# Kernel optimization log

Measured on AMD Instinct MI355X. Metric: run time of the kernel, lower is better.

## Reference

```python
import jax, jax.numpy as jnp
import numpy as np
from jax import lax

D = 384      # embd_d
L = 4        # num_blocks
B = 64
SHW, THW = 24, 12
NS, NT = SHW * SHW, THW * THW   # 576, 144
EPS = 1e-5


def _ln(x, g, b):
    mu = jnp.mean(x, axis=-1, keepdims=True)
    var = jnp.mean(jnp.square(x - mu), axis=-1, keepdims=True)
    return (x - mu) * lax.rsqrt(var + EPS) * g + b


def setup_inputs() -> dict:
    key = jax.random.key(0)
    ks = iter(jax.random.split(key, 64))
    f32 = jnp.float32
    def nrm(shape, s=0.02):
        return jax.random.normal(next(ks), shape, dtype=f32) * s
    inp = {
        'search': jax.random.normal(next(ks), (B, NS, D), dtype=f32),
        'target': jax.random.normal(next(ks), (B, NT, D), dtype=f32),
        # learned tokens / positional params
        'cls': nrm((1, 1, D), 1.0),
        'search_pos': nrm((1, NS, D), 0.5),
        'target_pos': nrm((1, NT, D), 0.5),
        # stacked per-block params [L, ...]
        'ln1_g': jnp.ones((L, D), f32), 'ln1_b': jnp.zeros((L, D), f32),
        'Wq': nrm((L, D, D)), 'bq': jnp.zeros((L, D), f32),
        'Wk': nrm((L, D, D)), 'bk': jnp.zeros((L, D), f32),
        'Wv': nrm((L, D, D)), 'bv': jnp.zeros((L, D), f32),
        'ln2_g': jnp.ones((L, D), f32), 'ln2_b': jnp.zeros((L, D), f32),
        'W1': nrm((L, D, 2 * D)), 'b1': jnp.zeros((L, 2 * D), f32),
        'W2': nrm((L, 2 * D, D)), 'b2': jnp.zeros((L, D), f32),
        # head
        'lnf_g': jnp.ones((D,), f32), 'lnf_b': jnp.zeros((D,), f32),
        'Wl1': nrm((D, D)), 'bl1': jnp.zeros((D,), f32),
        'Wl2': nrm((D, 1)), 'bl2': jnp.zeros((1,), f32),
    }
    return inp


def reference(search, target, cls, search_pos, target_pos,
              ln1_g, ln1_b, Wq, bq, Wk, bk, Wv, bv,
              ln2_g, ln2_b, W1, b1, W2, b2,
              lnf_g, lnf_b, Wl1, bl1, Wl2, bl2):
    scale = D ** (-0.5)  # note: full embed dim, as in source
    x = jnp.concatenate([
        jnp.broadcast_to(cls, (B, 1, D)),
        search + search_pos,
        target + target_pos,
    ], axis=1)  # [B, 1+Ns+Nt, D]

    def block(x, p):
        l1g, l1b, wq, bq_, wk, bk_, wv, bv_, l2g, l2b, w1, b1_, w2, b2_ = p
        y = _ln(x, l1g, l1b)
        q = y @ wq + bq_
        k = y @ wk + bk_
        v = y @ wv + bv_
        attn = jax.nn.softmax(jnp.einsum('bid,bjd->bij', q, k) * scale, axis=-1)
        x = x + jnp.einsum('bij,bjd->bid', attn, v)
        h = _ln(x, l2g, l2b)
        x = x + (jax.nn.gelu(h @ w1 + b1_, approximate=False) @ w2 + b2_)
        return x, None

    x, _ = lax.scan(block, x, (ln1_g, ln1_b, Wq, bq, Wk, bk, Wv, bv,
                               ln2_g, ln2_b, W1, b1, W2, b2))
    h = _ln(x[:, 0], lnf_g, lnf_b)          # cls token [B, D]
    h = jax.nn.relu(h @ Wl1 + bl1)
    return h @ Wl2 + bl2                     # [B, 1]
```

## Files before the change

### kernel.cpp

```cpp
#include <hip/hip_runtime.h>
#include <hip/hip_bf16.h>
#include <math.h>

#define DD 384
#define NBATCH 64
#define NSEQ 721
#define NROWS (NBATCH*NSEQ)
#define NLAYER 4

typedef __bf16 bf16_t;
typedef __bf16 bf16x8 __attribute__((ext_vector_type(8)));
typedef float  f32x4  __attribute__((ext_vector_type(4)));

static __device__ __forceinline__ void split_bf16(float v, bf16_t& h, bf16_t& l) {
    h = (bf16_t)v;
    l = (bf16_t)(v - (float)h);
}
static __device__ __forceinline__ bf16x8 bzero8() {
    bf16x8 v = {(bf16_t)0.f,(bf16_t)0.f,(bf16_t)0.f,(bf16_t)0.f,
                (bf16_t)0.f,(bf16_t)0.f,(bf16_t)0.f,(bf16_t)0.f};
    return v;
}
static __device__ __forceinline__ void gload16(const void* g, void* l) {
    __builtin_amdgcn_global_load_lds(
        (const __attribute__((address_space(1))) unsigned int*)g,
        (__attribute__((address_space(3))) unsigned int*)l, 16, 0, 0);
}
static __device__ __forceinline__ int xcd_swz(int nwg) {
    int orig = blockIdx.x;
    int q = nwg >> 3, r = nwg & 7;
    int xcd = orig & 7, within = orig >> 3;
    int base = (xcd < r) ? xcd*(q+1) : r*(q+1) + (xcd - r)*q;
    return base + within;
}
static __device__ __forceinline__ void ln_from_partials(const float* ss, const float* ss2,
                                                        int row, float& mu, float& rstd) {
    float s = 0.f, q2 = 0.f;
    #pragma unroll
    for (int k = 0; k < 6; ++k) { s += ss[k*NROWS + row]; q2 += ss2[k*NROWS + row]; }
    mu = s * (1.f/DD);
    float var = q2 * (1.f/DD) - mu*mu;
    rstd = rsqrtf(var + 1e-5f);
}

__global__ __launch_bounds__(256) void build_x_kernel(const float* __restrict__ search,
                               const float* __restrict__ target,
                               const float* __restrict__ cls,
                               const float* __restrict__ spos,
                               const float* __restrict__ tpos,
                               bf16_t* __restrict__ xh, bf16_t* __restrict__ xl,
                               float* __restrict__ wss, float* __restrict__ wss2) {
    int wave = threadIdx.x >> 6, lane = threadIdx.x & 63;
    int row = blockIdx.x * 4 + wave;
    if (row >= NROWS) return;
    int b = row / NSEQ, n = row % NSEQ;
    float s = 0.f, q2 = 0.f;
    #pragma unroll
    for (int i = 0; i < 6; ++i) {
        int d = lane + 64*i;
        float val;
        if (n == 0)        val = cls[d];
        else if (n <= 576) val = search[((size_t)b*576 + (n-1))*DD + d] + spos[(size_t)(n-1)*DD + d];
        else               val = target[((size_t)b*144 + (n-577))*DD + d] + tpos[(size_t)(n-577)*DD + d];
        bf16_t h, l;
        split_bf16(val, h, l);
        xh[(size_t)row*DD + d] = h;
        xl[(size_t)row*DD + d] = l;
        s += val; q2 += val*val;
    }
    #pragma unroll
    for (int m = 1; m < 64; m <<= 1) { s += __shfl_xor(s, m); q2 += __shfl_xor(q2, m); }
    if (lane == 0) {
        wss[row] = s; wss2[row] = q2;
        #pragma unroll
        for (int k = 1; k < 6; ++k) { wss[k*NROWS + row] = 0.f; wss2[k*NROWS + row] = 0.f; }
    }
}

__global__ void transpose_split_kernel(const float* __restrict__ src,
                                       const float* __restrict__ g,
                                       bf16_t* __restrict__ dh,
                                       bf16_t* __restrict__ dl,
                                       int K, int N) {
    int idx = blockIdx.x * blockDim.x + threadIdx.x;
    if (idx >= K*N) return;
    int k = idx / N, n = idx % N;
    float v = src[idx];
    if (g) v *= g[k];
    bf16_t h, l;
    split_bf16(v, h, l);
    dh[(size_t)n*K + k] = h;
    dl[(size_t)n*K + k] = l;
}

__global__ void colsum_kernel(const float* __restrict__ W, const float* __restrict__ g,
                              const float* __restrict__ b, const float* __restrict__ bias,
                              float* __restrict__ c1, float* __restrict__ c2,
                              int K, int N, int outStride, int outOff) {
    int l = blockIdx.y;
    int n = blockIdx.x * 256 + threadIdx.x;
    if (n >= N) return;
    const float* Wl = W + (size_t)l*K*N;
    const float* gl = g + (size_t)l*K;
    const float* bl = b + (size_t)l*K;
    float s1 = 0.f, s2 = 0.f;
    for (int k = 0; k < K; ++k) {
        float w = Wl[(size_t)k*N + n];
        s1 = fmaf(gl[k], w, s1);
        s2 = fmaf(bl[k], w, s2);
    }
    c1[(size_t)l*outStride + outOff + n] = s1;
    c2[(size_t)l*outStride + outOff + n] = s2 + bias[(size_t)l*N + n];
}

static __device__ __forceinline__ void gemm_core(
        const bf16_t* __restrict__ ah, const bf16_t* __restrict__ al,
        const bf16_t* __restrict__ bh, const bf16_t* __restrict__ bl,
        bf16_t (&ls)[32][64][8],
        int m0, int n0, int K, f32x4 (&acc)[4][4]) {
    int t = threadIdx.x;
    int w = t >> 6, lane = t & 63;
    int c = lane & 15, g = lane >> 4;
    int wr = w >> 1, wc = w & 1;
    const bf16_t* src0 = (w==0) ? ah : (w==1) ? al : (w==2) ? bh : bl;
    int base_rc = (w < 2) ? m0 : n0;
    const bf16_t* srcbase = src0 + (size_t)(base_rc + c)*K + 8*g;

    int ksteps = K >> 5;
    for (int kt = 0; kt < ksteps; ++kt) {
        int k0 = kt << 5;
        __syncthreads();
        #pragma unroll
        for (int i = 0; i < 8; ++i)
            gload16(srcbase + (size_t)(16*i)*K + k0, &ls[w*8 + i][0][0]);
        __syncthreads();
        bf16x8 af_h[4], af_l[4], bf_h[4], bf_l[4];
        #pragma unroll
        for (int i = 0; i < 4; ++i) {
            af_h[i] = *(const bf16x8*)&ls[     4*wr + i][lane][0];
            af_l[i] = *(const bf16x8*)&ls[ 8 + 4*wr + i][lane][0];
            bf_h[i] = *(const bf16x8*)&ls[16 + 4*wc + i][lane][0];
            bf_l[i] = *(const bf16x8*)&ls[24 + 4*wc + i][lane][0];
        }
        #pragma unroll
        for (int i = 0; i < 4; ++i)
            #pragma unroll
            for (int j = 0; j < 4; ++j) {
                acc[i][j] = __builtin_amdgcn_mfma_f32_16x16x32_bf16(af_h[i], bf_h[j], acc[i][j], 0,0,0);
                acc[i][j] = __builtin_amdgcn_mfma_f32_16x16x32_bf16(af_h[i], bf_l[j], acc[i][j], 0,0,0);
                acc[i][j] = __builtin_amdgcn_mfma_f32_16x16x32_bf16(af_l[i], bf_h[j], acc[i][j], 0,0,0);
            }
    }
}

__global__ __launch_bounds__(256, 4) void gemm_qkv(
        const bf16_t* __restrict__ ah, const bf16_t* __restrict__ al,
        const bf16_t* __restrict__ bh, const bf16_t* __restrict__ bl,
        const float* __restrict__ ss, const float* __restrict__ ss2,
        const float* __restrict__ c1, const float* __restrict__ c2,
        bf16_t* __restrict__ qout, bf16_t* __restrict__ kout,
        bf16_t* __restrict__ vth, bf16_t* __restrict__ vtl,
        int M, int MP, int nwg) {
    __shared__ __align__(16) bf16_t ls[32][64][8];
    int wgid = xcd_swz(nwg);
    int m0 = (wgid / 9) * 128, n0 = (wgid % 9) * 128;
    f32x4 zero4 = {0.f,0.f,0.f,0.f};
    f32x4 acc[4][4];
    #pragma unroll
    for (int i = 0; i < 4; ++i)
        #pragma unroll
        for (int j = 0; j < 4; ++j) acc[i][j] = zero4;
    gemm_core(ah, al, bh, bl, ls, m0, n0, DD, acc);

    int t = threadIdx.x, w = t >> 6, lane = t & 63;
    int c = lane & 15, g = lane >> 4;
    int wr = w >> 1, wc = w & 1;
    float rmu[16], rrs[16];
    #pragma unroll
    for (int i = 0; i < 4; ++i)
        #pragma unroll
        for (int r = 0; r < 4; ++r) {
            int row = m0 + 64*wr + 16*i + 4*g + r;
            float mu = 0.f, rstd = 1.f;
            if (row < M) ln_from_partials(ss, ss2, row, mu, rstd);
            rmu[i*4+r] = mu; rrs[i*4+r] = rstd;
        }
    int seg = n0 / 384;
    if (seg < 2) {
        bf16_t* outb = (seg == 0) ? qout : kout;
        int segoff = seg * 384;
        #pragma unroll
        for (int j = 0; j < 4; ++j) {
            int nglob = n0 + 64*wc + 16*j + c;
            int nloc = nglob - segoff;
            float C1 = c1[nglob], C2 = c2[nglob];
            #pragma unroll
            for (int i = 0; i < 4; ++i) {
                int rbase = m0 + 64*wr + 16*i + 4*g;
                #pragma unroll
                for (int r = 0; r < 4; ++r) {
                    int row = rbase + r;
                    if (row >= M) continue;
                    float val = rrs[i*4+r]*(acc[i][j][r] - rmu[i*4+r]*C1) + C2;
                    outb[(size_t)row*DD + nloc] = (bf16_t)val;
                }
            }
        }
    } else {
        int vbase = n0 - 768;
        bool tail = (m0 + 128 > M);
        if (!tail) {
            bf16_t* LST = &ls[0][0][0];
            #pragma unroll
            for (int pass = 0; pass < 2; ++pass) {
                __syncthreads();
                #pragma unroll
                for (int j = 0; j < 4; ++j) {
                    int d = 64*wc + 16*j + c;
                    int nglob = 768 + vbase + 0; (void)nglob;
                    float C1 = c1[n0 + 64*wc + 16*j + c];
                    float C2 = c2[n0 + 64*wc + 16*j + c];
                    #pragma unroll
                    for (int i = 0; i < 4; ++i)
                        #pragma unroll
                        for (int r = 0; r < 4; ++r) {
                            int tok = 64*wr + 16*i + 4*g + r;
                            float val = rrs[i*4+r]*(acc[i][j][r] - rmu[i*4+r]*C1) + C2;
                            bf16_t h, l;
                            split_bf16(val, h, l);
                            LST[d*128 + (tok ^ ((d & 15) << 3))] = pass ? l : h;
                        }
                }
                __syncthreads();
                bf16_t* outp = pass ? vtl : vth;
                #pragma unroll
                for (int p = 0; p < 8; ++p) {
                    int chunk = t + 256*p;
                    int d = chunk >> 4;
                    int tok0 = (chunk & 15) * 8;
                    uint4 v = *(const uint4*)&LST[d*128 + (tok0 ^ ((d & 15) << 3))];
                    *(uint4*)(outp + (size_t)(vbase + d)*MP + m0 + tok0) = v;
                }
            }
        } else {
            #pragma unroll
            for (int j = 0; j < 4; ++j) {
                int d = vbase + 64*wc + 16*j + c;
                float C1 = c1[n0 + 64*wc + 16*j + c];
                float C2 = c2[n0 + 64*wc + 16*j + c];
                #pragma unroll
                for (int i = 0; i < 4; ++i) {
                    int rbase = m0 + 64*wr + 16*i + 4*g;
                    #pragma unroll
                    for (int r = 0; r < 4; ++r) {
                        int row = rbase + r;
                        if (row >= M) continue;
                        float val = rrs[i*4+r]*(acc[i][j][r] - rmu[i*4+r]*C1) + C2;
                        bf16_t h, l;
                        split_bf16(val, h, l);
                        size_t o = (size_t)d*MP + row;
                        vth[o] = h;
                        vtl[o] = l;
                    }
                }
            }
        }
    }
}

template<int EPI, int NT>
__global__ __launch_bounds__(256, 4) void gemm_mfma(
        const bf16_t* __restrict__ ah, const bf16_t* __restrict__ al,
        const bf16_t* __restrict__ bh, const bf16_t* __restrict__ bl,
        const float* __restrict__ ss, const float* __restrict__ ss2,
        const float* __restrict__ c1, const float* __restrict__ c2,
        const float* __restrict__ bias,
        const bf16_t* __restrict__ resh, const bf16_t* __restrict__ resl,
        bf16_t* __restrict__ o1, bf16_t* __restrict__ o2,
        float* __restrict__ wss, float* __restrict__ wss2,
        int M, int N, int K, int nwg) {
    __shared__ __align__(16) bf16_t ls[32][64][8];
    int wgid = xcd_swz(nwg);
    int m0 = (wgid / NT) * 128, n0 = (wgid % NT) * 128;
    f32x4 zero4 = {0.f,0.f,0.f,0.f};
    f32x4 acc[4][4];
    #pragma unroll
    for (int i = 0; i < 4; ++i)
        #pragma unroll
        for (int j = 0; j < 4; ++j) acc[i][j] = zero4;
    gemm_core(ah, al, bh, bl, ls, m0, n0, K, acc);

    int t = threadIdx.x, w = t >> 6, lane = t & 63;
    int c = lane & 15, g = lane >> 4;
    int wr = w >> 1, wc = w & 1;

    if (EPI == 2) {
        float rmu[16], rrs[16];
        #pragma unroll
        for (int i = 0; i < 4; ++i)
            #pragma unroll
            for (int r = 0; r < 4; ++r) {
                int row = m0 + 64*wr + 16*i + 4*g + r;
                float mu = 0.f, rstd = 1.f;
                if (row < M) ln_from_partials(ss, ss2, row, mu, rstd);
                rmu[i*4+r] = mu; rrs[i*4+r] = rstd;
            }
        #pragma unroll
        for (int j = 0; j < 4; ++j) {
            int n = n0 + 64*wc + 16*j + c;
            float C1 = c1[n], C2 = c2[n];
            #pragma unroll
            for (int i = 0; i < 4; ++i) {
                int rbase = m0 + 64*wr + 16*i + 4*g;
                #pragma unroll
                for (int r = 0; r < 4; ++r) {
                    int row = rbase + r;
                    if (row >= M) continue;
                    float val = rrs[i*4+r]*(acc[i][j][r] - rmu[i*4+r]*C1) + C2;
                    val = 0.5f*val*(1.0f + erff(val*0.70710678118654752f));
                    bf16_t h, l;
                    split_bf16(val, h, l);
                    size_t o = (size_t)row*N + n;
                    o1[o] = h;
                    o2[o] = l;
                }
            }
        }
    } else {
        int slot = (wgid % NT) + 3*wc;
        #pragma unroll
        for (int i = 0; i < 4; ++i)
            #pragma unroll
            for (int r = 0; r < 4; ++r) {
                int row = m0 + 64*wr + 16*i + 4*g + r;
                if (row >= M) continue;
                float s = 0.f, q2 = 0.f;
                #pragma unroll
                for (int j = 0; j < 4; ++j) {
                    int n = n0 + 64*wc + 16*j + c;
                    size_t o = (size_t)row*N + n;
                    float val = acc[i][j][r] + bias[n] + (float)resh[o] + (float)resl[o];
                    bf16_t h, l;
                    split_bf16(val, h, l);
                    o1[o] = h;
                    o2[o] = l;
                    s += val; q2 += val*val;
                }
                #pragma unroll
                for (int m = 1; m < 16; m <<= 1) { s += __shfl_xor(s, m); q2 += __shfl_xor(q2, m); }
                if (c == 0) {
                    wss[slot*NROWS + row] = s;
                    wss2[slot*NROWS + row] = q2;
                }
            }
    }
}

__global__ __launch_bounds__(256, 2) void attn_mfma(
        const bf16_t* __restrict__ qh, const bf16_t* __restrict__ kh,
        const bf16_t* __restrict__ vth, const bf16_t* __restrict__ vtl,
        bf16_t* __restrict__ xh, bf16_t* __restrict__ xl,
        float* __restrict__ wss, float* __restrict__ wss2, int MP, int nwg) {
    __shared__ __align__(16) char smem[73728];
    bf16_t* kf = (bf16_t*)smem;
    char* vhp = smem + 24576;
    char* vlp = smem + 49152;

    int t = threadIdx.x, w = t >> 6, lane = t & 63;
    int c = lane & 15, g = lane >> 4;
    int wgid = xcd_swz(nwg);
    int bl_ = wgid / 12;
    int q0 = (wgid % 12) * 64;
    size_t bb = (size_t)bl_ * NSEQ;
    int qrow = q0 + 16*w + c;
    bool qok = (qrow < NSEQ);
    const float scale = 0.05103103630798287f;
    int vswz = (c ^ (c >> 2)) & 3;
    int dma_dd  = lane >> 2;
    int dma_kv8 = (lane & 3) ^ ((dma_dd ^ (dma_dd >> 2)) & 3);

    bf16x8 qf[12];
    #pragma unroll
    for (int ks = 0; ks < 12; ++ks) {
        if (qok) qf[ks] = *(const bf16x8*)(qh + (bb + qrow)*DD + 32*ks + 8*g);
        else     qf[ks] = bzero8();
    }

    f32x4 zero4 = {0.f,0.f,0.f,0.f};
    f32x4 oacc[24];
    #pragma unroll
    for (int i = 0; i < 24; ++i) oacc[i] = zero4;
    float m_run = -1e30f, l_run = 0.f;

    #pragma unroll
    for (int i = 0; i < 6; ++i) {
        int s = i*4 + w;
        int ks = s >> 1, mf = s & 1;
        gload16(kh + (bb + (size_t)(16*mf + c))*DD + 32*ks + 8*g, kf + s*512);
    }

    for (int kt = 0; kt < 23; ++kt) {
        int kv0 = kt * 32;
        asm volatile("s_waitcnt vmcnt(0)" ::: "memory");
        __builtin_amdgcn_s_barrier();
        #pragma unroll
        for (int i = 0; i < 6; ++i) {
            int s = i*4 + w;
            size_t gro = (size_t)(16*s + dma_dd)*MP + bb + kv0 + 8*dma_kv8;
            gload16(vth + gro, (bf16_t*)vhp + s*512);
            gload16(vtl + gro, (bf16_t*)vlp + s*512);
        }
        f32x4 sacc[2];
        sacc[0] = zero4; sacc[1] = zero4;
        #pragma unroll
        for (int ks = 0; ks < 12; ++ks) {
            bf16x8 a0 = *(const bf16x8*)(kf + ((size_t)(2*ks+0)*64 + lane)*8);
            bf16x8 a1 = *(const bf16x8*)(kf + ((size_t)(2*ks+1)*64 + lane)*8);
            sacc[0] = __builtin_amdgcn_mfma_f32_16x16x32_bf16(a0, qf[ks], sacc[0], 0,0,0);
            sacc[1] = __builtin_amdgcn_mfma_f32_16x16x32_bf16(a1, qf[ks], sacc[1], 0,0,0);
        }
        float p[2][4];
        float mx = -1e30f;
        #pragma unroll
        for (int mf = 0; mf < 2; ++mf)
            #pragma unroll
            for (int r = 0; r < 4; ++r) {
                float sv = sacc[mf][r] * scale;
                int kv = kv0 + 16*mf + 4*g + r;
                if (kv >= NSEQ) sv = -1e30f;
                p[mf][r] = sv;
                mx = fmaxf(mx, sv);
            }
        mx = fmaxf(mx, __shfl_xor(mx, 16));
        mx = fmaxf(mx, __shfl_xor(mx, 32));
        float m_new = fmaxf(m_run, mx);
        float corr = __expf(m_run - m_new);
        float psum = 0.f;
        #pragma unroll
        for (int mf = 0; mf < 2; ++mf)
            #pragma unroll
            for (int r = 0; r < 4; ++r) {
                float pv = __expf(p[mf][r] - m_new);
                p[mf][r] = pv;
                psum += pv;
            }
        psum += __shfl_xor(psum, 16);
        psum += __shfl_xor(psum, 32);
        l_run = l_run * corr + psum;
        m_run = m_new;
        #pragma unroll
        for (int i = 0; i < 24; ++i) oacc[i] *= corr;
        bf16x8 ph, pl;
        #pragma unroll
        for (int mf = 0; mf < 2; ++mf)
            #pragma unroll
            for (int r = 0; r < 4; ++r) {
                bf16_t hh, ll;
                split_bf16(p[mf][r], hh, ll);
                ph[mf*4 + r] = hh;
                pl[mf*4 + r] = ll;
            }
        asm volatile("s_waitcnt vmcnt(0)" ::: "memory");
        __builtin_amdgcn_s_barrier();
        if (kt + 1 < 23) {
            int kv0n = kv0 + 32;
            #pragma unroll
            for (int i = 0; i < 6; ++i) {
                int s = i*4 + w;
                int ks = s >> 1, mf = s & 1;
                gload16(kh + (bb + (size_t)(kv0n + 16*mf + c))*DD + 32*ks + 8*g, kf + s*512);
            }
        }
        #pragma unroll
        for (int mf = 0; mf < 24; ++mf) {
            int dr = 16*mf + c;
            const char* vb  = vhp + dr*64;
            const char* vb2 = vlp + dr*64;
            int o0 = ((((g>>1)     ^ vswz) << 4) | (8*(g&1)));
            int o1 = (((2 + (g>>1)) ^ vswz) << 4) | (8*(g&1));
            union { uint2 u[2]; bf16x8 v; } va, vc2;
            va.u[0]  = *(const uint2*)(vb  + o0);
            va.u[1]  = *(const uint2*)(vb  + o1);
            vc2.u[0] = *(const uint2*)(vb2 + o0);
            vc2.u[1] = *(const uint2*)(vb2 + o1);
            oacc[mf] = __builtin_amdgcn_mfma_f32_16x16x32_bf16(va.v,  ph, oacc[mf], 0,0,0);
            oacc[mf] = __builtin_amdgcn_mfma_f32_16x16x32_bf16(va.v,  pl, oacc[mf], 0,0,0);
            oacc[mf] = __builtin_amdgcn_mfma_f32_16x16x32_bf16(vc2.v, ph, oacc[mf], 0,0,0);
        }
    }
    float inv = 1.f / l_run;
    float s = 0.f, q2 = 0.f;
    if (qok) {
        bf16_t* xhr = xh + (bb + qrow)*DD;
        bf16_t* xlr = xl + (bb + qrow)*DD;
        #pragma unroll
        for (int mf = 0; mf < 24; ++mf)
            #pragma unroll
            for (int r = 0; r < 4; ++r) {
                int d = 16*mf + 4*g + r;
                float xv = (float)xhr[d] + (float)xlr[d] + oacc[mf][r]*inv;
                bf16_t h, l;
                split_bf16(xv, h, l);
                xhr[d] = h;
                xlr[d] = l;
                s += xv; q2 += xv*xv;
            }
    }
    s += __shfl_xor(s, 16);  q2 += __shfl_xor(q2, 16);
    s += __shfl_xor(s, 32);  q2 += __shfl_xor(q2, 32);
    if (qok && g == 0) {
        int rowL = bl_*NSEQ + qrow;
        wss[rowL] = s; wss2[rowL] = q2;
        #pragma unroll
        for (int k = 1; k < 6; ++k) { wss[k*NROWS + rowL] = 0.f; wss2[k*NROWS + rowL] = 0.f; }
    }
}

__global__ __launch_bounds__(384) void head_kernel(const bf16_t* __restrict__ xh,
    const bf16_t* __restrict__ xl,
    const float* __restrict__ g, const float* __restrict__ bb,
    const float* __restrict__ Wl1, const float* __restrict__ bl1,
    const float* __restrict__ Wl2, const float* __restrict__ bl2,
    float* __restrict__ outp) {
    __shared__ float yv[384];
    __shared__ float r1[6], r2[6], r3[6];
    int b = blockIdx.x, t = threadIdx.x;
    size_t o = (size_t)b*NSEQ*DD + t;
    float v = (float)xh[o] + (float)xl[o];
    float s = v;
    #pragma unroll
    for (int m = 1; m < 64; m <<= 1) s += __shfl_xor(s, m);
    if ((t & 63) == 0) r1[t>>6] = s;
    __syncthreads();
    float mu = (r1[0]+r1[1]+r1[2]+r1[3]+r1[4]+r1[5]) * (1.f/384.f);
    float dd = v - mu;
    float sq = dd*dd;
    #pragma unroll
    for (int m = 1; m < 64; m <<= 1) sq += __shfl_xor(sq, m);
    if ((t & 63) == 0) r2[t>>6] = sq;
    __syncthreads();
    float var = (r2[0]+r2[1]+r2[2]+r2[3]+r2[4]+r2[5]) * (1.f/384.f);
    float rstd = rsqrtf(var + 1e-5f);
    yv[t] = dd*rstd*g[t] + bb[t];
    __syncthreads();
    float acc = bl1[t];
    for (int d2 = 0; d2 < 384; d2++) acc = fmaf(yv[d2], Wl1[d2*384 + t], acc);
    acc = fmaxf(acc, 0.f);
    float oo = acc * Wl2[t];
    #pragma unroll
    for (int m = 1; m < 64; m <<= 1) oo += __shfl_xor(oo, m);
    if ((t & 63) == 0) r3[t>>6] = oo;
    __syncthreads();
    if (t == 0) outp[b] = r3[0]+r3[1]+r3[2]+r3[3]+r3[4]+r3[5] + bl2[0];
}

extern "C" void kernel_launch(void* const* d_in, const int* in_sizes, int n_in,
                              void* d_out, int out_size, void* d_ws, size_t ws_size,
                              hipStream_t stream) {
    const float* search = (const float*)d_in[0];
    const float* target = (const float*)d_in[1];
    const float* cls    = (const float*)d_in[2];
    const float* spos   = (const float*)d_in[3];
    const float* tpos   = (const float*)d_in[4];
    const float* ln1_g  = (const float*)d_in[5];
    const float* ln1_b  = (const float*)d_in[6];
    const float* Wq     = (const float*)d_in[7];
    const float* bq     = (const float*)d_in[8];
    const float* Wk     = (const float*)d_in[9];
    const float* bk     = (const float*)d_in[10];
    const float* Wv     = (const float*)d_in[11];
    const float* bv     = (const float*)d_in[12];
    const float* ln2_g  = (const float*)d_in[13];
    const float* ln2_b  = (const float*)d_in[14];
    const float* W1     = (const float*)d_in[15];
    const float* b1     = (const float*)d_in[16];
    const float* W2     = (const float*)d_in[17];
    const float* b2     = (const float*)d_in[18];
    const float* lnf_g  = (const float*)d_in[19];
    const float* lnf_b  = (const float*)d_in[20];
    const float* Wl1    = (const float*)d_in[21];
    const float* bl1    = (const float*)d_in[22];
    const float* Wl2    = (const float*)d_in[23];
    const float* bl2    = (const float*)d_in[24];

    size_t off = 0;
    char* base = (char*)d_ws;
    auto alloc = [&](size_t bytes) -> void* {
        void* p = base + off;
        off += (bytes + 255) & ~(size_t)255;
        return p;
    };

    bf16_t* xh = (bf16_t*)alloc((size_t)NROWS * DD * 2);
    bf16_t* xl = (bf16_t*)alloc((size_t)NROWS * DD * 2);
    float* ssum  = (float*)alloc((size_t)6*NROWS*4);
    float* ssum2 = (float*)alloc((size_t)6*NROWS*4);

    const int SQKV = 1152*DD;
    const int SM = DD*768;
    bf16_t* wqkvh = (bf16_t*)alloc((size_t)4*SQKV*2);
    bf16_t* wqkvl = (bf16_t*)alloc((size_t)4*SQKV*2);
    bf16_t* w1h = (bf16_t*)alloc((size_t)4*SM*2);
    bf16_t* w1l = (bf16_t*)alloc((size_t)4*SM*2);
    bf16_t* w2h = (bf16_t*)alloc((size_t)4*SM*2);
    bf16_t* w2l = (bf16_t*)alloc((size_t)4*SM*2);
    float* cqkv1 = (float*)alloc((size_t)4*1152*4);
    float* cqkv2 = (float*)alloc((size_t)4*1152*4);
    float* cm11  = (float*)alloc((size_t)4*768*4);
    float* cm12  = (float*)alloc((size_t)4*768*4);

    const size_t qB  = (size_t)NSEQ*DD*2;
    const size_t mB  = (size_t)NSEQ*768*2;
    const size_t perB = 2*qB + 4*(size_t)DD*NSEQ + 4096;
    size_t avail = (ws_size > off + 262144) ? (ws_size - off - 262144) : 0;
    int G = (int)(avail / perB);
    if (G > NBATCH) G = NBATCH;
    if (G < 1) G = 1;

    int MPi = (int)((((size_t)G*NSEQ + 7) & ~(size_t)7) + 32);
    size_t vBytes = (size_t)DD * MPi * 2;
    size_t sizeQKV = 2*qB*(size_t)G + 2*vBytes;
    size_t sizeMid = 2*mB*(size_t)G;
    size_t Usz = (sizeQKV > sizeMid ? sizeQKV : sizeMid);

    char* U = (char*)alloc(Usz);
    bf16_t* qhB  = (bf16_t*)U;
    bf16_t* khB  = (bf16_t*)(U + qB*G);
    bf16_t* vth  = (bf16_t*)(U + 2*qB*G);
    bf16_t* vtl  = (bf16_t*)(U + 2*qB*G + vBytes);
    bf16_t* midh = (bf16_t*)U;
    bf16_t* midl = (bf16_t*)(U + mB*G);

    build_x_kernel<<<(NROWS+3)/4, 256, 0, stream>>>(search, target, cls, spos, tpos,
                                                    xh, xl, ssum, ssum2);

    const int SQ = DD*DD;
    for (int l = 0; l < NLAYER; ++l) {
        bf16_t* dsth = wqkvh + (size_t)l*SQKV;
        bf16_t* dstl = wqkvl + (size_t)l*SQKV;
        transpose_split_kernel<<<(SQ+255)/256, 256, 0, stream>>>(Wq + (size_t)l*SQ, ln1_g + l*DD, dsth,          dstl,          DD, DD);
        transpose_split_kernel<<<(SQ+255)/256, 256, 0, stream>>>(Wk + (size_t)l*SQ, ln1_g + l*DD, dsth + 384*DD, dstl + 384*DD, DD, DD);
        transpose_split_kernel<<<(SQ+255)/256, 256, 0, stream>>>(Wv + (size_t)l*SQ, ln1_g + l*DD, dsth + 768*DD, dstl + 768*DD, DD, DD);
        transpose_split_kernel<<<(SM+255)/256, 256, 0, stream>>>(W1 + (size_t)l*SM, ln2_g + l*DD, w1h + (size_t)l*SM, w1l + (size_t)l*SM, DD, 768);
        transpose_split_kernel<<<(SM+255)/256, 256, 0, stream>>>(W2 + (size_t)l*SM, nullptr,      w2h + (size_t)l*SM, w2l + (size_t)l*SM, 768, DD);
    }
    colsum_kernel<<<dim3(2, NLAYER), 256, 0, stream>>>(Wq, ln1_g, ln1_b, bq, cqkv1, cqkv2, DD, DD, 1152, 0);
    colsum_kernel<<<dim3(2, NLAYER), 256, 0, stream>>>(Wk, ln1_g, ln1_b, bk, cqkv1, cqkv2, DD, DD, 1152, 384);
    colsum_kernel<<<dim3(2, NLAYER), 256, 0, stream>>>(Wv, ln1_g, ln1_b, bv, cqkv1, cqkv2, DD, DD, 1152, 768);
    colsum_kernel<<<dim3(3, NLAYER), 256, 0, stream>>>(W1, ln2_g, ln2_b, b1, cm11, cm12, DD, 768, 768, 0);

    for (int l = 0; l < NLAYER; ++l) {
        for (int b0 = 0; b0 < NBATCH; b0 += G) {
            int cb = (NBATCH - b0 < G) ? (NBATCH - b0) : G;
            int Mc = cb * NSEQ;
            bf16_t* xch = xh + (size_t)b0 * NSEQ * DD;
            bf16_t* xcl = xl + (size_t)b0 * NSEQ * DD;
            float* ssc  = ssum  + (size_t)b0 * NSEQ;
            float* ssc2 = ssum2 + (size_t)b0 * NSEQ;
            int mtiles = (Mc + 127)/128;
            int nwgQKV = 9*mtiles, nwgM1 = 6*mtiles, nwgM2 = 3*mtiles, nwgA = 12*cb;

            gemm_qkv<<<nwgQKV, 256, 0, stream>>>(xch, xcl,
                    wqkvh + (size_t)l*SQKV, wqkvl + (size_t)l*SQKV,
                    ssc, ssc2, cqkv1 + l*1152, cqkv2 + l*1152,
                    qhB, khB, vth, vtl, Mc, MPi, nwgQKV);
            attn_mfma<<<nwgA, 256, 0, stream>>>(qhB, khB, vth, vtl, xch, xcl,
                    ssc, ssc2, MPi, nwgA);
            gemm_mfma<2,6><<<nwgM1, 256, 0, stream>>>(xch, xcl,
                    w1h + (size_t)l*SM, w1l + (size_t)l*SM,
                    ssc, ssc2, cm11 + l*768, cm12 + l*768, nullptr,
                    nullptr, nullptr, midh, midl, nullptr, nullptr, Mc, 768, DD, nwgM1);
            gemm_mfma<3,3><<<nwgM2, 256, 0, stream>>>(midh, midl,
                    w2h + (size_t)l*SM, w2l + (size_t)l*SM,
                    nullptr, nullptr, nullptr, nullptr, b2 + l*DD,
                    xch, xcl, xch, xcl, ssc, ssc2, Mc, DD, 768, nwgM2);
        }
    }
    head_kernel<<<NBATCH, 384, 0, stream>>>(xh, xl, lnf_g, lnf_b, Wl1, bl1, Wl2, bl2, (float*)d_out);
}
```

Measured before the change: 4.044 ms.

## Tile QKV GEMM per batch and store V transposed per batch

The QKV GEMM now tiles the M dimension per batch element, using 6 tiles of 128 tokens over 721 tokens, and writes V transposed into a per-batch [DD][736] layout with zeroed padding. The old layout used one global transposed V with stride MP. Every tile now takes the coalesced LDS-transpose store path, and attention reads V using per-batch offsets. The cost is that per-batch tiles (768 rows for 721 tokens) do some wasted GEMM work, and the mid buffer sizing now relies on perB*G being large enough.

```diff
diff --git a/kernel.cpp b/kernel.cpp
--- a/kernel.cpp
+++ b/kernel.cpp
@@ -7,6 +7,7 @@
 #define NSEQ 721
 #define NROWS (NBATCH*NSEQ)
 #define NLAYER 4
+#define VTW 736
 
 typedef __bf16 bf16_t;
 typedef __bf16 bf16x8 __attribute__((ext_vector_type(8)));
@@ -160,17 +161,20 @@
         const float* __restrict__ c1, const float* __restrict__ c2,
         bf16_t* __restrict__ qout, bf16_t* __restrict__ kout,
         bf16_t* __restrict__ vth, bf16_t* __restrict__ vtl,
-        int M, int MP, int nwg) {
+        int nwg) {
     __shared__ __align__(16) bf16_t ls[32][64][8];
     int wgid = xcd_swz(nwg);
-    int m0 = (wgid / 9) * 128, n0 = (wgid % 9) * 128;
+    int mt = wgid / 9, n0 = (wgid % 9) * 128;
+    int blb = mt / 6;
+    int tok_base = (mt % 6) * 128;
+    int m0d = blb*NSEQ + tok_base;
     f32x4 zero4 = {0.f,0.f,0.f,0.f};
     f32x4 acc[4][4];
     #pragma unroll
     for (int i = 0; i < 4; ++i)
         #pragma unroll
         for (int j = 0; j < 4; ++j) acc[i][j] = zero4;
-    gemm_core(ah, al, bh, bl, ls, m0, n0, DD, acc);
+    gemm_core(ah, al, bh, bl, ls, m0d, n0, DD, acc);
 
     int t = threadIdx.x, w = t >> 6, lane = t & 63;
     int c = lane & 15, g = lane >> 4;
@@ -180,9 +184,9 @@
     for (int i = 0; i < 4; ++i)
         #pragma unroll
         for (int r = 0; r < 4; ++r) {
-            int row = m0 + 64*wr + 16*i + 4*g + r;
+            int tok = tok_base + 64*wr + 16*i + 4*g + r;
             float mu = 0.f, rstd = 1.f;
-            if (row < M) ln_from_partials(ss, ss2, row, mu, rstd);
+            if (tok < NSEQ) ln_from_partials(ss, ss2, blb*NSEQ + tok, mu, rstd);
             rmu[i*4+r] = mu; rrs[i*4+r] = rstd;
         }
     int seg = n0 / 384;
@@ -196,73 +200,49 @@
             float C1 = c1[nglob], C2 = c2[nglob];
             #pragma unroll
             for (int i = 0; i < 4; ++i) {
-                int rbase = m0 + 64*wr + 16*i + 4*g;
                 #pragma unroll
                 for (int r = 0; r < 4; ++r) {
-                    int row = rbase + r;
-                    if (row >= M) continue;
+                    int tok = tok_base + 64*wr + 16*i + 4*g + r;
+                    if (tok >= NSEQ) continue;
                     float val = rrs[i*4+r]*(acc[i][j][r] - rmu[i*4+r]*C1) + C2;
-                    outb[(size_t)row*DD + nloc] = (bf16_t)val;
+                    outb[(size_t)(blb*NSEQ + tok)*DD + nloc] = (bf16_t)val;
                 }
             }
         }
     } else {
         int vbase = n0 - 768;
-        bool tail = (m0 + 128 > M);
-        if (!tail) {
-            bf16_t* LST = &ls[0][0][0];
-            #pragma unroll
-            for (int pass = 0; pass < 2; ++pass) {
-                __syncthreads();
-                #pragma unroll
-                for (int j = 0; j < 4; ++j) {
-                    int d = 64*wc + 16*j + c;
-                    int nglob = 768 + vbase + 0; (void)nglob;
-                    float C1 = c1[n0 + 64*wc + 16*j + c];
-                    float C2 = c2[n0 + 64*wc + 16*j + c];
-                    #pragma unroll
-                    for (int i = 0; i < 4; ++i)
-                        #pragma unroll
-                        for (int r = 0; r < 4; ++r) {
-                            int tok = 64*wr + 16*i + 4*g + r;
-                            float val = rrs[i*4+r]*(acc[i][j][r] - rmu[i*4+r]*C1) + C2;
-                            bf16_t h, l;
-                            split_bf16(val, h, l);
-                            LST[d*128 + (tok ^ ((d & 15) << 3))] = pass ? l : h;
-                        }
-                }
-                __syncthreads();
-                bf16_t* outp = pass ? vtl : vth;
-                #pragma unroll
-                for (int p = 0; p < 8; ++p) {
-                    int chunk = t + 256*p;
-                    int d = chunk >> 4;
-                    int tok0 = (chunk & 15) * 8;
-                    uint4 v = *(const uint4*)&LST[d*128 + (tok0 ^ ((d & 15) << 3))];
-                    *(uint4*)(outp + (size_t)(vbase + d)*MP + m0 + tok0) = v;
-                }
-            }
-        } else {
+        bf16_t* LST = &ls[0][0][0];
+        #pragma unroll
+        for (int pass = 0; pass < 2; ++pass) {
+            __syncthreads();
             #pragma unroll
             for (int j = 0; j < 4; ++j) {
-                int d = vbase + 64*wc + 16*j + c;
+                int d = 64*wc + 16*j + c;
                 float C1 = c1[n0 + 64*wc + 16*j + c];
                 float C2 = c2[n0 + 64*wc + 16*j + c];
                 #pragma unroll
-                for (int i = 0; i < 4; ++i) {
-                    int rbase = m0 + 64*wr + 16*i + 4*g;
+                for (int i = 0; i < 4; ++i)
                     #pragma unroll
                     for (int r = 0; r < 4; ++r) {
-                        int row = rbase + r;
-                        if (row >= M) continue;
+                        int tokl = 64*wr + 16*i + 4*g + r;
                         float val = rrs[i*4+r]*(acc[i][j][r] - rmu[i*4+r]*C1) + C2;
+                        if (tok_base + tokl >= NSEQ) val = 0.f;
                         bf16_t h, l;
                         split_bf16(val, h, l);
-                        size_t o = (size_t)d*MP + row;
-                        vth[o] = h;
-                        vtl[o] = l;
+                        LST[d*128 + (tokl ^ ((d & 15) << 3))] = pass ? l : h;
                     }
-                }
+            }
+            __syncthreads();
+            bf16_t* outp = pass ? vtl : vth;
+            #pragma unroll
+            for (int p = 0; p < 8; ++p) {
+                int chunk = t + 256*p;
+                int d = chunk >> 4;
+                int tok0 = (chunk & 15) * 8;
+                int tg = tok_base + tok0;
+                if (tg + 8 > VTW) continue;
+                uint4 v = *(const uint4*)&LST[d*128 + (tok0 ^ ((d & 15) << 3))];
+                *(uint4*)(outp + ((size_t)(blb*DD + vbase + d))*VTW + tg) = v;
             }
         }
     }
@@ -360,7 +340,7 @@
         const bf16_t* __restrict__ qh, const bf16_t* __restrict__ kh,
         const bf16_t* __restrict__ vth, const bf16_t* __restrict__ vtl,
         bf16_t* __restrict__ xh, bf16_t* __restrict__ xl,
-        float* __restrict__ wss, float* __restrict__ wss2, int MP, int nwg) {
+        float* __restrict__ wss, float* __restrict__ wss2, int nwg) {
     __shared__ __align__(16) char smem[73728];
     bf16_t* kf = (bf16_t*)smem;
     char* vhp = smem + 24576;
@@ -406,7 +386,7 @@
         #pragma unroll
         for (int i = 0; i < 6; ++i) {
             int s = i*4 + w;
-            size_t gro = (size_t)(16*s + dma_dd)*MP + bb + kv0 + 8*dma_kv8;
+            size_t gro = ((size_t)(bl_*DD + 16*s + dma_dd))*VTW + kv0 + 8*dma_kv8;
             gload16(vth + gro, (bf16_t*)vhp + s*512);
             gload16(vtl + gro, (bf16_t*)vlp + s*512);
         }
@@ -610,24 +590,19 @@
     float* cm12  = (float*)alloc((size_t)4*768*4);
 
     const size_t qB  = (size_t)NSEQ*DD*2;
+    const size_t vB  = (size_t)DD*VTW*2;
     const size_t mB  = (size_t)NSEQ*768*2;
-    const size_t perB = 2*qB + 4*(size_t)DD*NSEQ + 4096;
+    const size_t perB = 2*qB + 2*vB;
     size_t avail = (ws_size > off + 262144) ? (ws_size - off - 262144) : 0;
     int G = (int)(avail / perB);
     if (G > NBATCH) G = NBATCH;
     if (G < 1) G = 1;
 
-    int MPi = (int)((((size_t)G*NSEQ + 7) & ~(size_t)7) + 32);
-    size_t vBytes = (size_t)DD * MPi * 2;
-    size_t sizeQKV = 2*qB*(size_t)G + 2*vBytes;
-    size_t sizeMid = 2*mB*(size_t)G;
-    size_t Usz = (sizeQKV > sizeMid ? sizeQKV : sizeMid);
-
-    char* U = (char*)alloc(Usz);
+    char* U = (char*)alloc(perB * G);
     bf16_t* qhB  = (bf16_t*)U;
     bf16_t* khB  = (bf16_t*)(U + qB*G);
     bf16_t* vth  = (bf16_t*)(U + 2*qB*G);
-    bf16_t* vtl  = (bf16_t*)(U + 2*qB*G + vBytes);
+    bf16_t* vtl  = (bf16_t*)(U + 2*qB*G + vB*G);
     bf16_t* midh = (bf16_t*)U;
     bf16_t* midl = (bf16_t*)(U + mB*G);
 
@@ -658,14 +633,14 @@
             float* ssc  = ssum  + (size_t)b0 * NSEQ;
             float* ssc2 = ssum2 + (size_t)b0 * NSEQ;
             int mtiles = (Mc + 127)/128;
-            int nwgQKV = 9*mtiles, nwgM1 = 6*mtiles, nwgM2 = 3*mtiles, nwgA = 12*cb;
+            int nwgQKV = 9*6*cb, nwgM1 = 6*mtiles, nwgM2 = 3*mtiles, nwgA = 12*cb;
 
             gemm_qkv<<<nwgQKV, 256, 0, stream>>>(xch, xcl,
                     wqkvh + (size_t)l*SQKV, wqkvl + (size_t)l*SQKV,
                     ssc, ssc2, cqkv1 + l*1152, cqkv2 + l*1152,
-                    qhB, khB, vth, vtl, Mc, MPi, nwgQKV);
+                    qhB, khB, vth, vtl, nwgQKV);
             attn_mfma<<<nwgA, 256, 0, stream>>>(qhB, khB, vth, vtl, xch, xcl,
-                    ssc, ssc2, MPi, nwgA);
+                    ssc, ssc2, nwgA);
             gemm_mfma<2,6><<<nwgM1, 256, 0, stream>>>(xch, xcl,
                     w1h + (size_t)l*SM, w1l + (size_t)l*SM,
                     ssc, ssc2, cm11 + l*768, cm12 + l*768, nullptr,
```

Measured after the change: 3.596 ms. -11.1%, faster.
